# Kernel optimization log

Measured on AMD Instinct MI355X. Metric: run time of the kernel, lower is better.

## Reference

```python
import jax, jax.numpy as jnp
import numpy as np

H = 16          # num_heads
W = 256         # sliding window size
LN_EPS = 1e-6
ROPE_BASE = 10000.0


def layer_norm(x, g, b):
    m = jnp.mean(x, axis=-1, keepdims=True)
    v = jnp.mean((x - m) ** 2, axis=-1, keepdims=True)
    return (x - m) * jax.lax.rsqrt(v + LN_EPS) * g + b


def rope(x):
    # x: [B, S, H, hd]; rotate-half RoPE
    S, hd = x.shape[1], x.shape[-1]
    inv_freq = 1.0 / (ROPE_BASE ** (jnp.arange(0, hd, 2, dtype=jnp.float32) / hd))
    ang = jnp.arange(S, dtype=jnp.float32)[:, None] * inv_freq[None, :]  # [S, hd/2]
    cos = jnp.concatenate([jnp.cos(ang), jnp.cos(ang)], axis=-1)[None, :, None, :]
    sin = jnp.concatenate([jnp.sin(ang), jnp.sin(ang)], axis=-1)[None, :, None, :]
    x1, x2 = jnp.split(x, 2, axis=-1)
    rot = jnp.concatenate([-x2, x1], axis=-1)
    return x * cos + rot * sin


def setup_inputs() -> dict:
    key = jax.random.key(0)
    ks = jax.random.split(key, 12)
    B, S, D, I = 2, 2048, 1024, 4096
    s = 0.02
    return {
        "hidden_states": jax.random.normal(ks[0], (B, S, D), jnp.float32),
        "wq": jax.random.normal(ks[1], (D, D), jnp.float32) * s,
        "wk": jax.random.normal(ks[2], (D, D), jnp.float32) * s,
        "wv": jax.random.normal(ks[3], (D, D), jnp.float32) * s,
        "wo": jax.random.normal(ks[4], (D, D), jnp.float32) * s,
        "w1": jax.random.normal(ks[5], (D, I), jnp.float32) * s,
        "w2": jax.random.normal(ks[6], (I, D), jnp.float32) * s,
        "w3": jax.random.normal(ks[7], (D, I), jnp.float32) * s,
        "ln1_g": jnp.ones((D,), jnp.float32),
        "ln1_b": jnp.zeros((D,), jnp.float32),
        "ln2_g": jnp.ones((D,), jnp.float32),
        "ln2_b": jnp.zeros((D,), jnp.float32),
    }


def reference(hidden_states, wq, wk, wv, wo, w1, w2, w3, ln1_g, ln1_b, ln2_g, ln2_b):
    B, S, D = hidden_states.shape
    hd = D // H

    # --- attention sub-block ---
    residual = hidden_states
    x = layer_norm(hidden_states, ln1_g, ln1_b)
    q = (x @ wq).reshape(B, S, H, hd)
    k = (x @ wk).reshape(B, S, H, hd)
    v = (x @ wv).reshape(B, S, H, hd)
    q, k = rope(q), rope(k)

    scores = jnp.einsum("bqhd,bkhd->bhqk", q, k) / jnp.sqrt(jnp.float32(hd))
    idx = jnp.arange(S)
    rel = idx[:, None] - idx[None, :]          # i - j
    mask = (rel >= 0) & (rel < W)              # causal sliding window
    scores = jnp.where(mask[None, None], scores, jnp.float32(-1e9))
    attn = jax.nn.softmax(scores, axis=-1)
    ctx = jnp.einsum("bhqk,bkhd->bqhd", attn, v).reshape(B, S, D)
    hidden_states = residual + ctx @ wo

    # --- SwiGLU MLP sub-block ---
    residual = hidden_states
    x = layer_norm(hidden_states, ln2_g, ln2_b)
    mlp = (jax.nn.silu(x @ w1) * (x @ w3)) @ w2
    return residual + mlp
```

## Files before the change

### kernel.cpp

```cpp
#include <hip/hip_runtime.h>
#include <hip/hip_bf16.h>

typedef __bf16 bf16_t;
typedef __bf16 bf16x4 __attribute__((ext_vector_type(4)));
typedef __bf16 bf16x8 __attribute__((ext_vector_type(8)));
typedef float f32x4 __attribute__((ext_vector_type(4)));

#define LN_EPS 1e-6f

__device__ __forceinline__ void gl2lds16(const void* g, void* l) {
    __builtin_amdgcn_global_load_lds(
        (const __attribute__((address_space(1))) void*)g,
        (__attribute__((address_space(3))) void*)l, 16, 0, 0);
}

__device__ __forceinline__ void block_sync() {
    __asm__ __volatile__("" ::: "memory");
    __builtin_amdgcn_s_barrier();
    __asm__ __volatile__("" ::: "memory");
}

__global__ void prep_weights_kernel(const float* __restrict__ wq, const float* __restrict__ wk,
                                    const float* __restrict__ wv, const float* __restrict__ wo,
                                    const float* __restrict__ w1, const float* __restrict__ w3,
                                    const float* __restrict__ w2, bf16_t* __restrict__ wq_t,
                                    bf16_t* __restrict__ wk_t, bf16_t* __restrict__ wv_t,
                                    bf16_t* __restrict__ wo_t, bf16_t* __restrict__ w13_t,
                                    bf16_t* __restrict__ w2_t) {
    __shared__ float tile[32][33];
    int id = blockIdx.x;
    const float* src;
    bf16_t* dst;
    int R, C, mode = 0;
    if (id < 4096) {
        int w = id >> 10;
        id &= 1023;
        src = (w == 0) ? wq : (w == 1) ? wk : (w == 2) ? wv : wo;
        dst = (w == 0) ? wq_t : (w == 1) ? wk_t : (w == 2) ? wv_t : wo_t;
        R = 1024; C = 1024;
    } else if (id < 8192) {
        id -= 4096; src = w1; dst = w13_t; R = 1024; C = 4096; mode = 1;
    } else if (id < 12288) {
        id -= 8192; src = w3; dst = w13_t; R = 1024; C = 4096; mode = 2;
    } else {
        id -= 12288; src = w2; dst = w2_t; R = 4096; C = 1024;
    }
    int tpc = C >> 5;
    int bx = id % tpc, by = id / tpc;
    int r0 = by * 32, c0 = bx * 32;
    int tx = threadIdx.x & 31;
    int ty = threadIdx.x >> 5;
#pragma unroll
    for (int i = 0; i < 4; i++) {
        int r = ty + i * 8;
        tile[r][tx] = src[(size_t)(r0 + r) * C + (c0 + tx)];
    }
    __syncthreads();
#pragma unroll
    for (int i = 0; i < 4; i++) {
        int r = ty + i * 8;
        int rr = c0 + r;
        if (mode) rr = ((rr >> 7) << 8) + (rr & 127) + ((mode == 2) ? 128 : 0);
        dst[(size_t)rr * R + (r0 + tx)] = (bf16_t)tile[tx][r];
    }
}

__global__ void ln_kernel(const float* __restrict__ x, const float* __restrict__ g,
                          const float* __restrict__ bb, bf16_t* __restrict__ out, int D) {
    int row = blockIdx.x;
    int t = threadIdx.x;
    const float4* xr = reinterpret_cast<const float4*>(x + (size_t)row * D);
    float4 v = xr[t];
    float s = v.x + v.y + v.z + v.w;
    __shared__ float sbuf[4];
    __shared__ float sbuf2[4];
    int wave = t >> 6, lane = t & 63;
#pragma unroll
    for (int o = 32; o > 0; o >>= 1) s += __shfl_xor(s, o);
    if (lane == 0) sbuf[wave] = s;
    __syncthreads();
    float mean = (sbuf[0] + sbuf[1] + sbuf[2] + sbuf[3]) / (float)D;
    float d0 = v.x - mean, d1 = v.y - mean, d2 = v.z - mean, d3 = v.w - mean;
    float sq = d0 * d0 + d1 * d1 + d2 * d2 + d3 * d3;
#pragma unroll
    for (int o = 32; o > 0; o >>= 1) sq += __shfl_xor(sq, o);
    if (lane == 0) sbuf2[wave] = sq;
    __syncthreads();
    float var = (sbuf2[0] + sbuf2[1] + sbuf2[2] + sbuf2[3]) / (float)D;
    float inv = rsqrtf(var + LN_EPS);
    float4 gv = reinterpret_cast<const float4*>(g)[t];
    float4 bv = reinterpret_cast<const float4*>(bb)[t];
    bf16_t* o0 = out + (size_t)row * D + t * 4;
    o0[0] = (bf16_t)(d0 * inv * gv.x + bv.x);
    o0[1] = (bf16_t)(d1 * inv * gv.y + bv.y);
    o0[2] = (bf16_t)(d2 * inv * gv.z + bv.z);
    o0[3] = (bf16_t)(d3 * inv * gv.w + bv.w);
}

#define G4_BK 64

template <int EPI>
__launch_bounds__(256, 2) __global__
void gemm4_kernel(const bf16_t* __restrict__ A, const bf16_t* __restrict__ Bt,
                  float* __restrict__ Cf, const float* __restrict__ aux,
                  const bf16_t* __restrict__ auxb, bf16_t* __restrict__ Cb,
                  int M, int N, int K, int lda, int ldb) {
    __shared__ __align__(16) bf16_t As[128 * G4_BK];
    __shared__ __align__(16) bf16_t Bs[128 * G4_BK];
    const int t = threadIdx.x;
    const int wave = t >> 6, lane = t & 63;
    const int lr = lane & 15, quad = lane >> 4;
    const int wm = (wave >> 1) * 64, wn = (wave & 1) * 64;

    const int gx = gridDim.x, gy = gridDim.y;
    const int nwg = gx * gy;
    const int lin = blockIdx.y * gx + blockIdx.x;
    const int qch = nwg >> 3;
    const int sw = (lin & 7) * qch + (lin >> 3);
    const int m0 = (sw / gy) * 128;
    const int n0 = (sw % gy) * 128;
    const int koff = blockIdx.z * K;

    const int srow = t >> 3;
    const int sslot = (t & 7) ^ (srow & 7);
    const bf16_t* agp = A + (size_t)(m0 + srow) * lda + koff + sslot * 8;
    const bf16_t* bgp = Bt + (size_t)(n0 + srow) * ldb + koff + sslot * 8;
    bf16_t* asl = As + t * 8;
    bf16_t* bsl = Bs + t * 8;

    int aoff[4][2], boff[4][2];
#pragma unroll
    for (int f = 0; f < 4; f++)
#pragma unroll
        for (int s = 0; s < 2; s++) {
            int ra = wm + f * 16 + lr;
            int rb = wn + f * 16 + lr;
            aoff[f][s] = ra * G4_BK + (((s * 4 + quad) ^ (ra & 7)) << 3);
            boff[f][s] = rb * G4_BK + (((s * 4 + quad) ^ (rb & 7)) << 3);
        }

    f32x4 acc[4][4];
#pragma unroll
    for (int mi = 0; mi < 4; mi++)
#pragma unroll
        for (int ni = 0; ni < 4; ni++) acc[mi][ni] = 0.f;

    for (int k0 = 0; k0 < K; k0 += G4_BK) {
#pragma unroll
        for (int i = 0; i < 4; i++)
            gl2lds16(agp + k0 + (size_t)(32 * i) * lda, asl + i * 2048);
#pragma unroll
        for (int i = 0; i < 4; i++)
            gl2lds16(bgp + k0 + (size_t)(32 * i) * ldb, bsl + i * 2048);
        __syncthreads();
#pragma unroll
        for (int s = 0; s < 2; s++) {
            bf16x8 af[4], bfv[4];
#pragma unroll
            for (int mi = 0; mi < 4; mi++)
                af[mi] = *reinterpret_cast<const bf16x8*>(&As[aoff[mi][s]]);
#pragma unroll
            for (int ni = 0; ni < 4; ni++)
                bfv[ni] = *reinterpret_cast<const bf16x8*>(&Bs[boff[ni][s]]);
#pragma unroll
            for (int mi = 0; mi < 4; mi++)
#pragma unroll
                for (int ni = 0; ni < 4; ni++)
                    acc[mi][ni] = __builtin_amdgcn_mfma_f32_16x16x32_bf16(af[mi], bfv[ni],
                                                                          acc[mi][ni], 0, 0, 0);
        }
        __syncthreads();
    }

#pragma unroll
    for (int mi = 0; mi < 4; mi++)
#pragma unroll
        for (int ni = 0; ni < 4; ni++)
#pragma unroll
            for (int j = 0; j < 4; j++) {
                int gm = m0 + wm + mi * 16 + quad * 4 + j;
                int gn = n0 + wn + ni * 16 + lr;
                size_t idx = (size_t)gm * N + gn;
                float val = acc[mi][ni][j];
                if constexpr (EPI == 1) {
                    Cf[idx] = val + aux[idx];
                }
            }
}


__device__ __forceinline__ void stage_half(const bf16_t* g, int ld, bf16_t* l,
                                           int wave, int lane) {
#pragma unroll
    for (int i = 0; i < 2; i++) {
        int lidx = (wave * 2 + i) * 64 + lane;
        int row = lidx >> 3;
        int ss = (lidx & 7) ^ (row & 7);
        gl2lds16(g + (size_t)row * ld + ss * 8, l + (wave * 2 + i) * 512);
    }
}

template <int QM, int QN>
__device__ __forceinline__ void quad_mfma(f32x4 (&acc)[2][2][4][2], const bf16x8 (&af)[4][2],
                                          const bf16x8 (&bf)[2][2]) {
#pragma unroll
    for (int fr = 0; fr < 4; fr++)
#pragma unroll
        for (int fc = 0; fc < 2; fc++)
#pragma unroll
            for (int ks = 0; ks < 2; ks++)
                acc[QM][QN][fr][fc] = __builtin_amdgcn_mfma_f32_16x16x32_bf16(
                    af[fr][ks], bf[fc][ks], acc[QM][QN][fr][fc], 0, 0, 0);
}

template <int EPI>
__launch_bounds__(512, 2) __global__
void gemm6_kernel(const bf16_t* __restrict__ A, const bf16_t* __restrict__ Bt,
                  const bf16_t* __restrict__ auxb, bf16_t* __restrict__ Cb,
                  bf16_t* __restrict__ Cb2, int M, int N, int K, int lda, int ldb) {
    extern __shared__ __align__(16) bf16_t smem[];
    bf16_t* smA = smem;
    bf16_t* smB = smem + 32768;
    const int t = threadIdx.x;
    const int wave = t >> 6, lane = t & 63;
    const int lr = lane & 15, quad = lane >> 4;
    const int rowgrp = wave >> 2;
    const int colgrp = wave & 3;
    const int cg1 = colgrp & 1, cg2 = colgrp >> 1;

    const int gx = gridDim.x, gy = gridDim.y;
    const int nwg = gx * gy;
    const int lin = blockIdx.y * gx + blockIdx.x;
    const int qch = nwg >> 3;
    const int sw = (lin & 7) * qch + (lin >> 3);
    const int m0 = (sw / gy) * 256;
    const int n0 = (sw % gy) * 256;
    const int koff = blockIdx.z * K;

    const bf16_t* Ag = A + (size_t)m0 * lda + koff;
    const bf16_t* Bg = Bt + (size_t)n0 * ldb + koff;

    int aoff[4][2], boff[2][2];
#pragma unroll
    for (int fr = 0; fr < 4; fr++)
#pragma unroll
        for (int ks = 0; ks < 2; ks++) {
            int ra = rowgrp * 64 + fr * 16 + lr;
            aoff[fr][ks] = ra * 64 + (((ks * 4 + quad) ^ (ra & 7)) << 3);
        }
#pragma unroll
    for (int fc = 0; fc < 2; fc++)
#pragma unroll
        for (int ks = 0; ks < 2; ks++) {
            int rb = cg1 * 64 + cg2 * 16 + fc * 32 + lr;
            boff[fc][ks] = rb * 64 + (((ks * 4 + quad) ^ (rb & 7)) << 3);
        }

    f32x4 acc[2][2][4][2];
#pragma unroll
    for (int qm = 0; qm < 2; qm++)
#pragma unroll
        for (int qn = 0; qn < 2; qn++)
#pragma unroll
            for (int fr = 0; fr < 4; fr++)
#pragma unroll
                for (int fc = 0; fc < 2; fc++) acc[qm][qn][fr][fc] = 0.f;

    const int NT = K >> 6;

    stage_half(Ag, lda, smA, wave, lane);
    stage_half(Bg, ldb, smB, wave, lane);
    stage_half(Bg + (size_t)128 * ldb, ldb, smB + 8192, wave, lane);
    stage_half(Ag + (size_t)128 * lda, lda, smA + 8192, wave, lane);
    if (NT > 1) {
        stage_half(Ag + 64, lda, smA + 16384, wave, lane);
        __asm__ __volatile__("s_waitcnt vmcnt(2)" ::: "memory");
    } else {
        __asm__ __volatile__("s_waitcnt vmcnt(0)" ::: "memory");
    }
    block_sync();

    bf16x8 af[4][2], bf0[2][2], bf1[2][2];

    for (int tt = 0; tt < NT; ++tt) {
        const int cur = tt & 1, nxt = cur ^ 1;
        const bf16_t* A0b = smA + cur * 16384;
        const bf16_t* A1b = A0b + 8192;
        const bf16_t* B0b = smB + cur * 16384;
        const bf16_t* B1b = B0b + 8192;
        bf16_t* sAn = smA + nxt * 16384;
        bf16_t* sBn = smB + nxt * 16384;
        bf16_t* sAc = smA + cur * 16384;
        const bool pf1 = (tt + 1 < NT);
        const bool pf2 = (tt + 2 < NT);
        const size_t kn1 = (size_t)(tt + 1) << 6;
        const size_t kn2 = (size_t)(tt + 2) << 6;

#pragma unroll
        for (int fr = 0; fr < 4; fr++)
#pragma unroll
            for (int ks = 0; ks < 2; ks++)
                af[fr][ks] = *reinterpret_cast<const bf16x8*>(A0b + aoff[fr][ks]);
#pragma unroll
        for (int fc = 0; fc < 2; fc++)
#pragma unroll
            for (int ks = 0; ks < 2; ks++)
                bf0[fc][ks] = *reinterpret_cast<const bf16x8*>(B0b + boff[fc][ks]);
        if (pf1) stage_half(Bg + kn1, ldb, sBn, wave, lane);
        block_sync();
        __asm__ __volatile__("s_waitcnt lgkmcnt(0)" ::: "memory");
        __builtin_amdgcn_sched_barrier(0);
        __builtin_amdgcn_s_setprio(1);
        quad_mfma<0, 0>(acc, af, bf0);
        __builtin_amdgcn_s_setprio(0);
        block_sync();

#pragma unroll
        for (int fc = 0; fc < 2; fc++)
#pragma unroll
            for (int ks = 0; ks < 2; ks++)
                bf1[fc][ks] = *reinterpret_cast<const bf16x8*>(B1b + boff[fc][ks]);
        if (pf1) stage_half(Bg + (size_t)128 * ldb + kn1, ldb, sBn + 8192, wave, lane);
        block_sync();
        __asm__ __volatile__("s_waitcnt lgkmcnt(0)" ::: "memory");
        __builtin_amdgcn_sched_barrier(0);
        __builtin_amdgcn_s_setprio(1);
        quad_mfma<0, 1>(acc, af, bf1);
        __builtin_amdgcn_s_setprio(0);
        block_sync();

#pragma unroll
        for (int fr = 0; fr < 4; fr++)
#pragma unroll
            for (int ks = 0; ks < 2; ks++)
                af[fr][ks] = *reinterpret_cast<const bf16x8*>(A1b + aoff[fr][ks]);
        if (pf1) stage_half(Ag + (size_t)128 * lda + kn1, lda, sAn + 8192, wave, lane);
        block_sync();
        __asm__ __volatile__("s_waitcnt lgkmcnt(0)" ::: "memory");
        __builtin_amdgcn_sched_barrier(0);
        __builtin_amdgcn_s_setprio(1);
        quad_mfma<1, 1>(acc, af, bf1);
        __builtin_amdgcn_s_setprio(0);
        block_sync();

        if (pf2) stage_half(Ag + kn2, lda, sAc, wave, lane);
        __builtin_amdgcn_s_setprio(1);
        quad_mfma<1, 0>(acc, af, bf0);
        __builtin_amdgcn_s_setprio(0);
        __asm__ __volatile__("s_waitcnt vmcnt(2)" ::: "memory");
        block_sync();
    }

    if constexpr (EPI == 3) {
        if (n0 < 2048) {
            const float kfreq = -0.41524101186f;
            const int d = cg2 * 16 + lr;
            const float freq = exp2f((float)d * kfreq);
#pragma unroll
            for (int qm = 0; qm < 2; qm++)
#pragma unroll
                for (int qn = 0; qn < 2; qn++) {
                    const int gnb = n0 + qn * 128 + cg1 * 64;
#pragma unroll
                    for (int fr = 0; fr < 4; fr++)
#pragma unroll
                        for (int j = 0; j < 4; j++) {
                            int gm = m0 + qm * 128 + rowgrp * 64 + fr * 16 + quad * 4 + j;
                            float pos = (float)(gm & 2047);
                            float ang = pos * freq;
                            float sn, cs;
                            __sincosf(ang, &sn, &cs);
                            float x1 = acc[qm][qn][fr][0][j];
                            float x2 = acc[qm][qn][fr][1][j];
                            size_t idx = (size_t)gm * N + gnb + d;
                            Cb[idx] = (bf16_t)(x1 * cs - x2 * sn);
                            Cb[idx + 32] = (bf16_t)(x2 * cs + x1 * sn);
                        }
                }
        } else {
#pragma unroll
            for (int qm = 0; qm < 2; qm++)
#pragma unroll
                for (int qn = 0; qn < 2; qn++)
#pragma unroll
                    for (int fr = 0; fr < 4; fr++)
#pragma unroll
                        for (int fc = 0; fc < 2; fc++) {
                            int gmb = m0 + qm * 128 + rowgrp * 64 + fr * 16 + quad * 4;
                            int vcol = (n0 - 2048) + qn * 128 + cg1 * 64 + cg2 * 16 + fc * 32 + lr;
                            int hh = vcol >> 6, dd = vcol & 63;
                            int bb2 = gmb >> 11, ss = gmb & 2047;
                            bf16x4 pk;
#pragma unroll
                            for (int j = 0; j < 4; j++) pk[j] = (bf16_t)acc[qm][qn][fr][fc][j];
                            *reinterpret_cast<bf16x4*>(
                                &Cb2[(((size_t)(bb2 * 16 + hh)) * 64 + dd) * 2048 + ss]) = pk;
                        }
        }
    } else if constexpr (EPI == 6) {
        const int No = N >> 1;
#pragma unroll
        for (int qm = 0; qm < 2; qm++)
#pragma unroll
            for (int fr = 0; fr < 4; fr++)
#pragma unroll
                for (int fc = 0; fc < 2; fc++)
#pragma unroll
                    for (int j = 0; j < 4; j++) {
                        int gm = m0 + qm * 128 + rowgrp * 64 + fr * 16 + quad * 4 + j;
                        int c = (n0 >> 1) + cg1 * 64 + cg2 * 16 + fc * 32 + lr;
                        float a = acc[qm][0][fr][fc][j];
                        float bv = acc[qm][1][fr][fc][j];
                        float sl = a / (1.0f + __expf(-a));
                        Cb[(size_t)gm * No + c] = (bf16_t)(sl * bv);
                    }
    } else {
        size_t outoff = (EPI == 5) ? (size_t)blockIdx.z * M * N : 0;
#pragma unroll
        for (int qm = 0; qm < 2; qm++)
#pragma unroll
            for (int qn = 0; qn < 2; qn++)
#pragma unroll
                for (int fr = 0; fr < 4; fr++)
#pragma unroll
                    for (int fc = 0; fc < 2; fc++)
#pragma unroll
                        for (int j = 0; j < 4; j++) {
                            int gm = m0 + qm * 128 + rowgrp * 64 + fr * 16 + quad * 4 + j;
                            int gn = n0 + qn * 128 + cg1 * 64 + cg2 * 16 + fc * 32 + lr;
                            size_t idx = (size_t)gm * N + gn;
                            float val = acc[qm][qn][fr][fc][j];
                            if constexpr (EPI == 5) {
                                Cb[outoff + idx] = (bf16_t)val;
                            } else {
                                Cb[idx] = (bf16_t)val;
                            }
                        }
    }
}

__global__ void reduce4_kernel(const bf16_t* __restrict__ p, const float* __restrict__ hid,
                               float* __restrict__ out, int n4) {
    int i = blockIdx.x * 256 + threadIdx.x;
    if (i >= n4) return;
    size_t i4 = (size_t)i * 4;
    float4 h = *reinterpret_cast<const float4*>(hid + i4);
    const size_t stride = (size_t)4096 * 1024;
#pragma unroll
    for (int c = 0; c < 4; c++) {
        bf16x4 a = *reinterpret_cast<const bf16x4*>(p + c * stride + i4);
        h.x += (float)a[0];
        h.y += (float)a[1];
        h.z += (float)a[2];
        h.w += (float)a[3];
    }
    *reinterpret_cast<float4*>(out + i4) = h;
}

#define PSTR 40
#define QKVS 3072
__global__ __launch_bounds__(256, 2) void attn_kernel(const bf16_t* __restrict__ qkv,
                                                      const bf16_t* __restrict__ vt,
                                                      bf16_t* __restrict__ ctx, int S) {
    __shared__ __align__(16) bf16_t Pbuf[4][16 * PSTR];
    int t = threadIdx.x;
    int wave = t >> 6, lane = t & 63;
    int col = lane & 15, quad = lane >> 4;
    int h = blockIdx.y, b = blockIdx.z;
    int q0 = blockIdx.x * 64 + wave * 16;

    const bf16_t* qrow = qkv + (size_t)(b * S + q0 + col) * QKVS + h * 64;
    bf16x8 aq0 = *reinterpret_cast<const bf16x8*>(qrow + quad * 8);
    bf16x8 aq1 = *reinterpret_cast<const bf16x8*>(qrow + 32 + quad * 8);

    int jbase = q0 - 256;
    f32x4 sc[17];
#pragma unroll
    for (int kt = 0; kt < 17; kt++) {
        int j = jbase + kt * 16 + col;
        int jc = j < 0 ? 0 : (j > S - 1 ? S - 1 : j);
        const bf16_t* krow = qkv + (size_t)(b * S + jc) * QKVS + 1024 + h * 64;
        bf16x8 bk0 = *reinterpret_cast<const bf16x8*>(krow + quad * 8);
        bf16x8 bk1 = *reinterpret_cast<const bf16x8*>(krow + 32 + quad * 8);
        f32x4 c0 = {0.f, 0.f, 0.f, 0.f};
        c0 = __builtin_amdgcn_mfma_f32_16x16x32_bf16(aq0, bk0, c0, 0, 0, 0);
        c0 = __builtin_amdgcn_mfma_f32_16x16x32_bf16(aq1, bk1, c0, 0, 0, 0);
        sc[kt] = c0;
    }
#pragma unroll
    for (int kt = 0; kt < 17; kt++) {
#pragma unroll
        for (int jj = 0; jj < 4; jj++) {
            int qq = quad * 4 + jj;
            int j = jbase + kt * 16 + col;
            int rel = (q0 + qq) - j;
            bool ok = (j >= 0) && (rel >= 0) && (rel < 256);
            sc[kt][jj] = ok ? sc[kt][jj] * 0.125f : -1e30f;
        }
    }
    float sminv[4];
#pragma unroll
    for (int jj = 0; jj < 4; jj++) {
        float m = -1e30f;
#pragma unroll
        for (int kt = 0; kt < 17; kt++) m = fmaxf(m, sc[kt][jj]);
#pragma unroll
        for (int o = 1; o < 16; o <<= 1) m = fmaxf(m, __shfl_xor(m, o));
        float s = 0.f;
#pragma unroll
        for (int kt = 0; kt < 17; kt++) {
            float p = __expf(sc[kt][jj] - m);
            sc[kt][jj] = p;
            s += p;
        }
#pragma unroll
        for (int o = 1; o < 16; o <<= 1) s += __shfl_xor(s, o);
        sminv[jj] = 1.0f / s;
    }
    f32x4 o[4];
#pragma unroll
    for (int n = 0; n < 4; n++) o[n] = 0.f;
    bf16_t* myP = Pbuf[wave];
    const bf16_t* vplane = vt + ((size_t)(b * 16 + h)) * 64 * S;
#pragma unroll
    for (int c = 0; c < 9; c++) {
#pragma unroll
        for (int half = 0; half < 2; half++) {
            int kt = 2 * c + half;
#pragma unroll
            for (int jj = 0; jj < 4; jj++) {
                int qq = quad * 4 + jj;
                bf16_t pv = (kt < 17) ? (bf16_t)(sc[kt < 17 ? kt : 0][jj] * sminv[jj])
                                      : (bf16_t)0.f;
                myP[qq * PSTR + half * 16 + col] = pv;
            }
        }
        bf16x8 ap = *reinterpret_cast<const bf16x8*>(myP + col * PSTR + quad * 8);
        int key0 = jbase + c * 32 + quad * 8;
        int kc = key0 < 0 ? 0 : (key0 > S - 8 ? S - 8 : key0);
#pragma unroll
        for (int n = 0; n < 4; n++) {
            bf16x8 bv = *reinterpret_cast<const bf16x8*>(vplane + ((size_t)(n * 16 + col)) * S + kc);
            o[n] = __builtin_amdgcn_mfma_f32_16x16x32_bf16(ap, bv, o[n], 0, 0, 0);
        }
    }
#pragma unroll
    for (int n = 0; n < 4; n++)
#pragma unroll
        for (int jj = 0; jj < 4; jj++) {
            int qq = quad * 4 + jj;
            ctx[((size_t)(b * S + q0 + qq) * 16 + h) * 64 + n * 16 + col] = (bf16_t)o[n][jj];
        }
}

extern "C" void kernel_launch(void* const* d_in, const int* in_sizes, int n_in,
                              void* d_out, int out_size, void* d_ws, size_t ws_size,
                              hipStream_t stream) {
    const float* hs   = (const float*)d_in[0];
    const float* wq   = (const float*)d_in[1];
    const float* wk   = (const float*)d_in[2];
    const float* wv   = (const float*)d_in[3];
    const float* wo   = (const float*)d_in[4];
    const float* w1   = (const float*)d_in[5];
    const float* w2   = (const float*)d_in[6];
    const float* w3   = (const float*)d_in[7];
    const float* ln1g = (const float*)d_in[8];
    const float* ln1b = (const float*)d_in[9];
    const float* ln2g = (const float*)d_in[10];
    const float* ln2b = (const float*)d_in[11];
    float* out = (float*)d_out;

    const int B = 2, S = 2048, D = 1024, I = 4096;
    const int BS = B * S;

    char* ws = (char*)d_ws;
    const size_t MB = 1024 * 1024;
    bf16_t* wq_t  = (bf16_t*)(ws + 0 * MB);
    bf16_t* wk_t  = (bf16_t*)(ws + 2 * MB);
    bf16_t* wv_t  = (bf16_t*)(ws + 4 * MB);
    bf16_t* wo_t  = (bf16_t*)(ws + 6 * MB);
    bf16_t* w13_t = (bf16_t*)(ws + 8 * MB);
    bf16_t* w2_t  = (bf16_t*)(ws + 24 * MB);
    bf16_t* x_b   = (bf16_t*)(ws + 32 * MB);
    float*  hid   = (float*)(ws + 40 * MB);
    bf16_t* x2_b  = (bf16_t*)(ws + 56 * MB);
    bf16_t* qkvb  = (bf16_t*)(ws + 64 * MB);
    bf16_t* vt    = (bf16_t*)(ws + 88 * MB);
    bf16_t* ctxb  = (bf16_t*)(ws + 96 * MB);
    bf16_t* hbuf  = (bf16_t*)(ws + 96 * MB);
    bf16_t* pker  = (bf16_t*)(ws + 64 * MB);

    hipFuncSetAttribute(reinterpret_cast<const void*>(&gemm6_kernel<3>),
                        hipFuncAttributeMaxDynamicSharedMemorySize, 131072);
    hipFuncSetAttribute(reinterpret_cast<const void*>(&gemm6_kernel<5>),
                        hipFuncAttributeMaxDynamicSharedMemorySize, 131072);
    hipFuncSetAttribute(reinterpret_cast<const void*>(&gemm6_kernel<6>),
                        hipFuncAttributeMaxDynamicSharedMemorySize, 131072);

    dim3 tb(256);
    dim3 tb6(512);

    prep_weights_kernel<<<dim3(16384), tb, 0, stream>>>(wq, wk, wv, wo, w1, w3, w2, wq_t, wk_t,
                                                        wv_t, wo_t, w13_t, w2_t);

    ln_kernel<<<BS, tb, 0, stream>>>(hs, ln1g, ln1b, x_b, D);

    gemm6_kernel<3><<<dim3(BS / 256, 3072 / 256), tb6, 131072, stream>>>(
        x_b, wq_t, nullptr, qkvb, vt, BS, 3072, D, D, D);

    attn_kernel<<<dim3(S / 64, 16, B), tb, 0, stream>>>(qkvb, vt, ctxb, S);

    gemm4_kernel<1><<<dim3(BS / 128, D / 128), tb, 0, stream>>>(
        ctxb, wo_t, hid, hs, nullptr, nullptr, BS, D, D, D, D);

    ln_kernel<<<BS, tb, 0, stream>>>(hid, ln2g, ln2b, x2_b, D);

    gemm6_kernel<6><<<dim3(BS / 256, 8192 / 256), tb6, 131072, stream>>>(
        x2_b, w13_t, nullptr, hbuf, nullptr, BS, 8192, D, D, D);

    gemm6_kernel<5><<<dim3(BS / 256, D / 256, 4), tb6, 131072, stream>>>(
        hbuf, w2_t, nullptr, pker, nullptr, BS, D, 1024, I, I);
    reduce4_kernel<<<dim3(BS * D / 4 / 256), tb, 0, stream>>>(pker, hid, out, BS * D / 4);
}
```

Before: 356.0 us.

## Restructure GEMM main loop: fewer barriers, incremental pointers, unrolled double-buffer pipeline

```diff
diff --git a/kernel.cpp b/kernel.cpp
--- a/kernel.cpp
+++ b/kernel.cpp
@@ -189,17 +189,6 @@
 }
 
 
-__device__ __forceinline__ void stage_half(const bf16_t* g, int ld, bf16_t* l,
-                                           int wave, int lane) {
-#pragma unroll
-    for (int i = 0; i < 2; i++) {
-        int lidx = (wave * 2 + i) * 64 + lane;
-        int row = lidx >> 3;
-        int ss = (lidx & 7) ^ (row & 7);
-        gl2lds16(g + (size_t)row * ld + ss * 8, l + (wave * 2 + i) * 512);
-    }
-}
-
 template <int QM, int QN>
 __device__ __forceinline__ void quad_mfma(f32x4 (&acc)[2][2][4][2], const bf16x8 (&af)[4][2],
                                           const bf16x8 (&bf)[2][2]) {
@@ -240,6 +229,25 @@
     const bf16_t* Ag = A + (size_t)m0 * lda + koff;
     const bf16_t* Bg = Bt + (size_t)n0 * ldb + koff;
 
+    const int li0 = (wave * 2 + 0) * 64 + lane;
+    const int li1 = (wave * 2 + 1) * 64 + lane;
+    const int r0s = li0 >> 3, c0s = ((li0 & 7) ^ (r0s & 7)) << 3;
+    const int r1s = li1 >> 3, c1s = ((li1 & 7) ^ (r1s & 7)) << 3;
+    const bf16_t* pA0[2] = {Ag + (size_t)r0s * lda + c0s, Ag + (size_t)r1s * lda + c1s};
+    const bf16_t* pA1[2] = {pA0[0] + (size_t)128 * lda, pA0[1] + (size_t)128 * lda};
+    const bf16_t* pB0[2] = {Bg + (size_t)r0s * ldb + c0s, Bg + (size_t)r1s * ldb + c1s};
+    const bf16_t* pB1[2] = {pB0[0] + (size_t)128 * ldb, pB0[1] + (size_t)128 * ldb};
+    const int dl0 = (wave * 2 + 0) * 512;
+    const int dl1 = (wave * 2 + 1) * 512;
+
+#define STG(P, LBASE)                          \
+    do {                                       \
+        gl2lds16(P[0], (LBASE) + dl0);         \
+        P[0] += 64;                            \
+        gl2lds16(P[1], (LBASE) + dl1);         \
+        P[1] += 64;                            \
+    } while (0)
+
     int aoff[4][2], boff[2][2];
 #pragma unroll
     for (int fr = 0; fr < 4; fr++)
@@ -268,88 +276,72 @@
 
     const int NT = K >> 6;
 
-    stage_half(Ag, lda, smA, wave, lane);
-    stage_half(Bg, ldb, smB, wave, lane);
-    stage_half(Bg + (size_t)128 * ldb, ldb, smB + 8192, wave, lane);
-    stage_half(Ag + (size_t)128 * lda, lda, smA + 8192, wave, lane);
-    if (NT > 1) {
-        stage_half(Ag + 64, lda, smA + 16384, wave, lane);
-        __asm__ __volatile__("s_waitcnt vmcnt(2)" ::: "memory");
-    } else {
-        __asm__ __volatile__("s_waitcnt vmcnt(0)" ::: "memory");
-    }
+    STG(pA0, smA);
+    STG(pB0, smB);
+    STG(pB1, smB + 8192);
+    STG(pA1, smA + 8192);
+    STG(pA0, smA + 16384);
+    __asm__ __volatile__("s_waitcnt vmcnt(2)" ::: "memory");
     block_sync();
 
     bf16x8 af[4][2], bf0[2][2], bf1[2][2];
 
-    for (int tt = 0; tt < NT; ++tt) {
-        const int cur = tt & 1, nxt = cur ^ 1;
-        const bf16_t* A0b = smA + cur * 16384;
-        const bf16_t* A1b = A0b + 8192;
-        const bf16_t* B0b = smB + cur * 16384;
-        const bf16_t* B1b = B0b + 8192;
-        bf16_t* sAn = smA + nxt * 16384;
-        bf16_t* sBn = smB + nxt * 16384;
-        bf16_t* sAc = smA + cur * 16384;
-        const bool pf1 = (tt + 1 < NT);
-        const bool pf2 = (tt + 2 < NT);
-        const size_t kn1 = (size_t)(tt + 1) << 6;
-        const size_t kn2 = (size_t)(tt + 2) << 6;
-
-#pragma unroll
-        for (int fr = 0; fr < 4; fr++)
-#pragma unroll
-            for (int ks = 0; ks < 2; ks++)
-                af[fr][ks] = *reinterpret_cast<const bf16x8*>(A0b + aoff[fr][ks]);
-#pragma unroll
-        for (int fc = 0; fc < 2; fc++)
-#pragma unroll
-            for (int ks = 0; ks < 2; ks++)
-                bf0[fc][ks] = *reinterpret_cast<const bf16x8*>(B0b + boff[fc][ks]);
-        if (pf1) stage_half(Bg + kn1, ldb, sBn, wave, lane);
-        block_sync();
-        __asm__ __volatile__("s_waitcnt lgkmcnt(0)" ::: "memory");
-        __builtin_amdgcn_sched_barrier(0);
-        __builtin_amdgcn_s_setprio(1);
-        quad_mfma<0, 0>(acc, af, bf0);
-        __builtin_amdgcn_s_setprio(0);
-        block_sync();
-
-#pragma unroll
-        for (int fc = 0; fc < 2; fc++)
-#pragma unroll
-            for (int ks = 0; ks < 2; ks++)
-                bf1[fc][ks] = *reinterpret_cast<const bf16x8*>(B1b + boff[fc][ks]);
-        if (pf1) stage_half(Bg + (size_t)128 * ldb + kn1, ldb, sBn + 8192, wave, lane);
-        block_sync();
-        __asm__ __volatile__("s_waitcnt lgkmcnt(0)" ::: "memory");
-        __builtin_amdgcn_sched_barrier(0);
-        __builtin_amdgcn_s_setprio(1);
-        quad_mfma<0, 1>(acc, af, bf1);
-        __builtin_amdgcn_s_setprio(0);
-        block_sync();
-
-#pragma unroll
-        for (int fr = 0; fr < 4; fr++)
-#pragma unroll
-            for (int ks = 0; ks < 2; ks++)
-                af[fr][ks] = *reinterpret_cast<const bf16x8*>(A1b + aoff[fr][ks]);
-        if (pf1) stage_half(Ag + (size_t)128 * lda + kn1, lda, sAn + 8192, wave, lane);
-        block_sync();
-        __asm__ __volatile__("s_waitcnt lgkmcnt(0)" ::: "memory");
-        __builtin_amdgcn_sched_barrier(0);
-        __builtin_amdgcn_s_setprio(1);
-        quad_mfma<1, 1>(acc, af, bf1);
-        __builtin_amdgcn_s_setprio(0);
-        block_sync();
-
-        if (pf2) stage_half(Ag + kn2, lda, sAc, wave, lane);
-        __builtin_amdgcn_s_setprio(1);
-        quad_mfma<1, 0>(acc, af, bf0);
-        __builtin_amdgcn_s_setprio(0);
-        __asm__ __volatile__("s_waitcnt vmcnt(2)" ::: "memory");
-        block_sync();
-    }
+#define BODY(CUR, STAGES)                                                              \
+    do {                                                                               \
+        const bf16_t* A0b = smA + (CUR) * 16384;                                       \
+        const bf16_t* A1b = A0b + 8192;                                                \
+        const bf16_t* B0b = smB + (CUR) * 16384;                                       \
+        const bf16_t* B1b = B0b + 8192;                                                \
+        bf16_t* nA = smA + (1 - (CUR)) * 16384;                                        \
+        bf16_t* nB = smB + (1 - (CUR)) * 16384;                                        \
+        _Pragma("unroll") for (int fr = 0; fr < 4; fr++)                               \
+            _Pragma("unroll") for (int ks = 0; ks < 2; ks++)                           \
+                af[fr][ks] = *reinterpret_cast<const bf16x8*>(A0b + aoff[fr][ks]);     \
+        _Pragma("unroll") for (int fc = 0; fc < 2; fc++)                               \
+            _Pragma("unroll") for (int ks = 0; ks < 2; ks++) {                         \
+            bf0[fc][ks] = *reinterpret_cast<const bf16x8*>(B0b + boff[fc][ks]);        \
+            bf1[fc][ks] = *reinterpret_cast<const bf16x8*>(B1b + boff[fc][ks]);        \
+        }                                                                              \
+        if ((STAGES) >= 1) STG(pB0, nB);                                               \
+        __asm__ __volatile__("s_waitcnt lgkmcnt(0)" ::: "memory");                     \
+        __builtin_amdgcn_sched_barrier(0);                                             \
+        __builtin_amdgcn_s_setprio(1);                                                 \
+        quad_mfma<0, 0>(acc, af, bf0);                                                 \
+        __builtin_amdgcn_s_setprio(0);                                                 \
+        if ((STAGES) >= 1) STG(pB1, nB + 8192);                                        \
+        __builtin_amdgcn_s_setprio(1);                                                 \
+        quad_mfma<0, 1>(acc, af, bf1);                                                 \
+        __builtin_amdgcn_s_setprio(0);                                                 \
+        _Pragma("unroll") for (int fr = 0; fr < 4; fr++)                               \
+            _Pragma("unroll") for (int ks = 0; ks < 2; ks++)                           \
+                af[fr][ks] = *reinterpret_cast<const bf16x8*>(A1b + aoff[fr][ks]);     \
+        if ((STAGES) >= 1) STG(pA1, nA + 8192);                                        \
+        __asm__ __volatile__("s_waitcnt lgkmcnt(0)" ::: "memory");                     \
+        __builtin_amdgcn_sched_barrier(0);                                             \
+        __builtin_amdgcn_s_setprio(1);                                                 \
+        quad_mfma<1, 1>(acc, af, bf1);                                                 \
+        quad_mfma<1, 0>(acc, af, bf0);                                                 \
+        __builtin_amdgcn_s_setprio(0);                                                 \
+        if ((STAGES) == 2) {                                                           \
+            block_sync();                                                              \
+            STG(pA0, smA + (CUR) * 16384);                                             \
+            __asm__ __volatile__("s_waitcnt vmcnt(2)" ::: "memory");                   \
+            block_sync();                                                              \
+        } else if ((STAGES) == 1) {                                                    \
+            __asm__ __volatile__("s_waitcnt vmcnt(0)" ::: "memory");                   \
+            block_sync();                                                              \
+        }                                                                              \
+    } while (0)
+
+    const int ND = (NT - 2) >> 1;
+    for (int it = 0; it < ND; ++it) {
+        BODY(0, 2);
+        BODY(1, 2);
+    }
+    BODY(0, 1);
+    BODY(1, 0);
+#undef BODY
+#undef STG
 
     if constexpr (EPI == 3) {
         if (n0 < 2048) {
```

After: 360.1 us. About the same (+1.2%).
